# Performance work log

Measured on AMD Instinct MI355X. Metric: run time of the kernel, lower is better.

The kernel has to match this reference:

```python
import jax, jax.numpy as jnp
import numpy as np

B, N, H, DH, E, D_IN = 2, 2048, 8, 32, 65536, 256
O = H * DH
SCALE = float(np.sqrt(DH))


def setup_inputs() -> dict:
    key = jax.random.key(0)
    ks = jax.random.split(key, 8)
    rng = np.random.default_rng(0)
    x = jax.random.normal(ks[0], (B, N, D_IN), jnp.float32)
    adj = jax.random.uniform(ks[1], (B, N, N), jnp.float32)
    # unique edges per graph so scatter-add matches torch advanced-index +=
    flat = np.stack([rng.choice(N * N, size=E, replace=False) for _ in range(B)])
    edge_index = jnp.asarray(np.stack([flat // N, flat % N], axis=1), jnp.int32)  # [B,2,E]
    edge_attr = jax.random.normal(ks[2], (B, E, H), jnp.float32)
    mask = jnp.ones((B, N), dtype=bool)
    qkv_w = jax.random.normal(ks[3], (D_IN, 3 * O), jnp.float32) / np.sqrt(D_IN)
    qkv_b = jnp.zeros((3 * O,), jnp.float32)
    e_w1 = jax.random.normal(ks[4], (H, H), jnp.float32) / np.sqrt(H)
    e_b1 = jnp.zeros((H,), jnp.float32)
    e_w2 = jax.random.normal(ks[5], (H, H), jnp.float32) / np.sqrt(H)
    e_b2 = jnp.zeros((H,), jnp.float32)
    shifts = jnp.asarray(np.linspace(0.1, 0.8, H), jnp.float32).reshape(1, H, 1, 1)
    widths = jnp.full((1, H, 1, 1), 0.5, jnp.float32)
    self_loop_W = jnp.asarray(1.0 / DH + rng.uniform(0, 1, H), jnp.float32).reshape(1, H, 1, 1)
    return dict(x=x, adj=adj, edge_attr=edge_attr, qkv_w=qkv_w, qkv_b=qkv_b,
                e_w1=e_w1, e_b1=e_b1, e_w2=e_w2, e_b2=e_b2,
                shifts=shifts, widths=widths, self_loop_W=self_loop_W,
                edge_index=edge_index, mask=mask)


def reference(x, adj, edge_attr, qkv_w, qkv_b, e_w1, e_b1, e_w2, e_b2,
              shifts, widths, self_loop_W, edge_index, mask):
    Bq, Nq = x.shape[0], x.shape[1]
    # qkv projection -> [3,B,H,N,DH]
    qkv = (x @ qkv_w + qkv_b).reshape(Bq, Nq, 3, H, DH)
    qkv = jnp.transpose(qkv, (2, 0, 3, 1, 4))
    Q, K, V = qkv[0], qkv[1], qkv[2]
    # edge FFN applied twice (eval mode: noise/dropout are identity)
    def ffn(e):
        return jax.nn.relu(e @ e_w1 + e_b1) @ e_w2 + e_b2
    ea = ffn(ffn(edge_attr))                      # [B,E,H]
    ea = jnp.transpose(ea, (0, 2, 1))             # [B,H,E]
    # scores + learned moire adjacency bias
    scores = jnp.einsum('bhqd,bhkd->bhqk', Q, K) / SCALE
    moire = jnp.exp(-((adj[:, None] - shifts) ** 2) / (2.0 * widths ** 2))  # gaussian focus
    moire = jnp.clip(moire, 1e-6, None)
    s = scores + jnp.log(moire)                   # [B,H,N,N]
    # scatter edge features into score matrix
    u = edge_index[:, 0, :]                        # [B,E]
    v = edge_index[:, 1, :]
    bi = jnp.arange(Bq)[:, None, None]
    hi = jnp.arange(H)[None, :, None]
    s = s.at[bi, hi, u[:, None, :], v[:, None, :]].add(ea)
    # self-loop diagonal bias (non-trainable)
    s = s + jnp.eye(Nq, dtype=s.dtype)[None, None] * self_loop_W
    # mask and softmax
    m2 = mask[:, None, :] & mask[:, :, None]       # [B,N,N]
    s = jnp.where(m2[:, None], s, jnp.asarray(-1e6, s.dtype))
    attn = jax.nn.softmax(s, axis=-1)
    out = jnp.einsum('bhqk,bhkd->bhqd', attn, V)
    return jnp.transpose(out, (0, 2, 1, 3)).reshape(Bq, Nq, O)
```

## Files before the change

kernel.cpp:

```cpp
#include <hip/hip_runtime.h>

#define B_ 2
#define N_ 2048
#define H_ 8
#define DH_ 32
#define E_ 65536
#define DIN_ 256
#define KT 256
#define PAD 4
#define ECAP 32
#define INV_SCALE 0.17677669529663687f
#define LOGMIN -13.815510557964274f

typedef short bf16x8 __attribute__((ext_vector_type(8)));
typedef float floatx4 __attribute__((ext_vector_type(4)));

__device__ __forceinline__ unsigned short f2b(float f){
  union { float f; unsigned int u; } v; v.f = f;
  return (unsigned short)((v.u + 0x7fffu + ((v.u >> 16) & 1u)) >> 16);
}
__device__ __forceinline__ bf16x8 f8_to_bf(const float* p){
  float4 a = *(const float4*)p, b = *(const float4*)(p + 4);
  bf16x8 r;
  r[0] = (short)f2b(a.x); r[1] = (short)f2b(a.y); r[2] = (short)f2b(a.z); r[3] = (short)f2b(a.w);
  r[4] = (short)f2b(b.x); r[5] = (short)f2b(b.y); r[6] = (short)f2b(b.z); r[7] = (short)f2b(b.w);
  return r;
}

__global__ __launch_bounds__(256) void prep_kernel(
    const float* __restrict__ eattr,
    const float* __restrict__ w1, const float* __restrict__ b1,
    const float* __restrict__ w2, const float* __restrict__ b2,
    float* __restrict__ ea,
    const int* __restrict__ ei, int* __restrict__ cnt, unsigned int* __restrict__ pck,
    const float* __restrict__ w, unsigned short* __restrict__ wT)
{
  int bb = blockIdx.x, tid = threadIdx.x;
  if (bb < 512){
    __shared__ float W1[64], W2[64], Bv1[8], Bv2[8];
    if (tid < 64){ W1[tid] = w1[tid]; W2[tid] = w2[tid]; }
    if (tid < 8){ Bv1[tid] = b1[tid]; Bv2[tid] = b2[tid]; }
    __syncthreads();
    int gid = bb * 256 + tid;
    const float* ep = eattr + (size_t)gid * 8;
    float cur[8];
#pragma unroll
    for (int i = 0; i < 8; ++i) cur[i] = ep[i];
#pragma unroll
    for (int pass = 0; pass < 2; ++pass){
      float t[8];
#pragma unroll
      for (int j = 0; j < 8; ++j){
        float s = Bv1[j];
#pragma unroll
        for (int i = 0; i < 8; ++i) s += cur[i] * W1[i * 8 + j];
        t[j] = fmaxf(s, 0.f);
      }
#pragma unroll
      for (int j = 0; j < 8; ++j){
        float s = Bv2[j];
#pragma unroll
        for (int i = 0; i < 8; ++i) s += t[i] * W2[i * 8 + j];
        cur[j] = s;
      }
    }
    float* op = ea + (size_t)gid * 8;
#pragma unroll
    for (int j = 0; j < 8; ++j) op[j] = cur[j];
  } else if (bb < 1024){
    int gid = (bb - 512) * 256 + tid;
    int b = gid >> 16, e = gid & (E_ - 1);
    int u = ei[(size_t)b * 2 * E_ + e];
    int v = ei[(size_t)b * 2 * E_ + E_ + e];
    int bucket = ((b << 11) + u) * 8 + (v >> 8);
    int slot = atomicAdd(&cnt[bucket], 1);
    if (slot < ECAP) pck[(size_t)bucket * ECAP + slot] = ((unsigned int)e << 11) | (unsigned int)v;
  } else {
    int k = bb - 1024;
    for (int c = tid; c < 768; c += 256)
      wT[(size_t)c * 256 + k] = f2b(w[(size_t)k * 768 + c]);
  }
}

__global__ __launch_bounds__(256) void qkv_kernel(
    const float* __restrict__ x, const unsigned short* __restrict__ wT,
    const float* __restrict__ bias,
    unsigned short* __restrict__ Qb, unsigned short* __restrict__ Kb, unsigned short* __restrict__ Vt)
{
  int tid = threadIdx.x;
  int wave = tid >> 6, lane = tid & 63, m = lane & 15, quad = lane >> 4;
  int rowbase = blockIdx.x * 16;
  int colbase = blockIdx.y * 64 + wave * 16;
  floatx4 acc = {0.f, 0.f, 0.f, 0.f};
#pragma unroll
  for (int kb = 0; kb < 8; ++kb){
    bf16x8 af = f8_to_bf(x + (size_t)(rowbase + m) * DIN_ + kb * 32 + quad * 8);
    bf16x8 bf = *(const bf16x8*)(wT + (size_t)(colbase + m) * DIN_ + kb * 32 + quad * 8);
    acc = __builtin_amdgcn_mfma_f32_16x16x32_bf16(af, bf, acc, 0, 0, 0);
  }
  int ccol = colbase + m;
  int which = ccol >> 8, hh = (ccol >> 5) & 7, dh = ccol & 31;
  float bv = bias[ccol];
#pragma unroll
  for (int r = 0; r < 4; ++r){
    int row = rowbase + quad * 4 + r;
    int bidx = row >> 11, n = row & (N_ - 1);
    float val = acc[r] + bv;
    size_t bh = (size_t)(bidx * H_ + hh);
    if (which == 0)      Qb[(bh * N_ + n) * DH_ + dh] = f2b(val * INV_SCALE);
    else if (which == 1) Kb[(bh * N_ + n) * DH_ + dh] = f2b(val);
    else                 Vt[(bh * DH_ + dh) * N_ + n] = f2b(val);
  }
}

__global__ __launch_bounds__(256) void attn_kernel(
    const unsigned short* __restrict__ Qb, const unsigned short* __restrict__ Kb,
    const unsigned short* __restrict__ Vt, const float* __restrict__ adj,
    const float* __restrict__ ea, const int* __restrict__ cnt, const unsigned int* __restrict__ pck,
    const float* __restrict__ shifts, const float* __restrict__ widths,
    const float* __restrict__ selfW, float* __restrict__ out)
{
  __shared__ float S[16][KT + PAD];
  __shared__ float mpart[4][16];
  __shared__ float mrowW[4][16];
  __shared__ float arowW[4][16];
  __shared__ float lfin[4][16];

  int bid = blockIdx.x;
  int qt = bid & 127, h = (bid >> 7) & 7, b = bid >> 10;
  int qbase = qt * 16;
  int tid = threadIdx.x, wave = tid >> 6, lane = tid & 63, m = lane & 15, quad = lane >> 4;
  float shift_h = shifts[h];
  float w_h = widths[h];
  float i2w_h = 1.f / (2.f * w_h * w_h);
  float selfW_h = selfW[h];
  size_t krow = (size_t)(b * H_ + h) * N_;
  size_t vrow = (size_t)(b * H_ + h) * DH_;
  bf16x8 qfrag = *(const bf16x8*)(Qb + (krow + qbase + m) * DH_ + quad * 8);

  float mcur = -1e30f;
  float lcur = 0.f;
  floatx4 oacc0 = {0.f, 0.f, 0.f, 0.f};
  floatx4 oacc1 = {0.f, 0.f, 0.f, 0.f};

  for (int kt = 0; kt < N_ / KT; ++kt){
    int k0 = kt * KT;
    bool diagtile = (k0 == (qbase & ~(KT - 1)));
#pragma unroll
    for (int s = 0; s < 4; ++s){
      int colofs = wave * 64 + s * 16;
      bf16x8 kf = *(const bf16x8*)(Kb + (krow + k0 + colofs + m) * DH_ + quad * 8);
      floatx4 acc = {0.f, 0.f, 0.f, 0.f};
      acc = __builtin_amdgcn_mfma_f32_16x16x32_bf16(qfrag, kf, acc, 0, 0, 0);
      int t = colofs + m - (qbase - k0);
#pragma unroll
      for (int r = 0; r < 4; ++r){
        float v = acc[r];
        if (diagtile && t == quad * 4 + r) v += selfW_h;
        S[quad * 4 + r][colofs + m] = v;
      }
    }
    __syncthreads();
#pragma unroll
    for (int ii = 0; ii < 4; ++ii){
      int i = tid + ii * 256;
      int r = i >> 6, c4 = (i & 63) << 2;
      float4 av = *(const float4*)(adj + ((size_t)b * N_ + qbase + r) * N_ + k0 + c4);
      float4* sp = (float4*)&S[r][c4];
      float4 sv = *sp;
      float d;
      d = av.x - shift_h; sv.x += fmaxf(-d * d * i2w_h, LOGMIN);
      d = av.y - shift_h; sv.y += fmaxf(-d * d * i2w_h, LOGMIN);
      d = av.z - shift_h; sv.z += fmaxf(-d * d * i2w_h, LOGMIN);
      d = av.w - shift_h; sv.w += fmaxf(-d * d * i2w_h, LOGMIN);
      *sp = sv;
    }
    __syncthreads();
#pragma unroll
    for (int ii = 0; ii < 2; ++ii){
      int i = tid + ii * 256;
      int r = i >> 5, slot = i & (ECAP - 1);
      int bucket = (b * N_ + qbase + r) * 8 + kt;
      int nb = cnt[bucket]; nb = nb > ECAP ? ECAP : nb;
      if (slot < nb){
        unsigned int p = pck[(size_t)bucket * ECAP + slot];
        int vv = (int)(p & (N_ - 1));
        int e  = (int)(p >> 11);
        S[r][vv - k0] += ea[((size_t)b * E_ + e) * H_ + h];
      }
    }
    __syncthreads();
    const float* sp0 = &S[m][wave * 64 + quad * 8];
    float4 s00 = *(const float4*)(sp0);
    float4 s01 = *(const float4*)(sp0 + 4);
    float4 s10 = *(const float4*)(sp0 + 32);
    float4 s11 = *(const float4*)(sp0 + 36);
    bf16x8 vf00 = *(const bf16x8*)(Vt + (vrow + m) * N_      + k0 + wave * 64 + quad * 8);
    bf16x8 vf01 = *(const bf16x8*)(Vt + (vrow + 16 + m) * N_ + k0 + wave * 64 + quad * 8);
    bf16x8 vf10 = *(const bf16x8*)(Vt + (vrow + m) * N_      + k0 + wave * 64 + 32 + quad * 8);
    bf16x8 vf11 = *(const bf16x8*)(Vt + (vrow + 16 + m) * N_ + k0 + wave * 64 + 32 + quad * 8);
    float lm = fmaxf(fmaxf(fmaxf(s00.x, s00.y), fmaxf(s00.z, s00.w)),
                     fmaxf(fmaxf(s01.x, s01.y), fmaxf(s01.z, s01.w)));
    lm = fmaxf(lm, fmaxf(fmaxf(fmaxf(s10.x, s10.y), fmaxf(s10.z, s10.w)),
                         fmaxf(fmaxf(s11.x, s11.y), fmaxf(s11.z, s11.w))));
    lm = fmaxf(lm, __shfl_xor(lm, 16));
    lm = fmaxf(lm, __shfl_xor(lm, 32));
    if (quad == 0) mpart[wave][m] = lm;
    __syncthreads();
    if (lane < 16){
      float tmax = fmaxf(fmaxf(mpart[0][lane], mpart[1][lane]),
                         fmaxf(mpart[2][lane], mpart[3][lane]));
      float mnew = fmaxf(mcur, tmax);
      float al = __expf(mcur - mnew);
      mcur = mnew;
      mrowW[wave][lane] = mnew;
      arowW[wave][lane] = al;
    }
    __threadfence_block();
    float mr  = mrowW[wave][m];
    float alA = arowW[wave][m];
    float4 aq = *(const float4*)&arowW[wave][quad * 4];
    oacc0[0] *= aq.x; oacc0[1] *= aq.y; oacc0[2] *= aq.z; oacc0[3] *= aq.w;
    oacc1[0] *= aq.x; oacc1[1] *= aq.y; oacc1[2] *= aq.z; oacc1[3] *= aq.w;
    float ps = 0.f, p;
    bf16x8 pf;
    p = __expf(s00.x - mr); ps += p; pf[0] = (short)f2b(p);
    p = __expf(s00.y - mr); ps += p; pf[1] = (short)f2b(p);
    p = __expf(s00.z - mr); ps += p; pf[2] = (short)f2b(p);
    p = __expf(s00.w - mr); ps += p; pf[3] = (short)f2b(p);
    p = __expf(s01.x - mr); ps += p; pf[4] = (short)f2b(p);
    p = __expf(s01.y - mr); ps += p; pf[5] = (short)f2b(p);
    p = __expf(s01.z - mr); ps += p; pf[6] = (short)f2b(p);
    p = __expf(s01.w - mr); ps += p; pf[7] = (short)f2b(p);
    oacc0 = __builtin_amdgcn_mfma_f32_16x16x32_bf16(pf, vf00, oacc0, 0, 0, 0);
    oacc1 = __builtin_amdgcn_mfma_f32_16x16x32_bf16(pf, vf01, oacc1, 0, 0, 0);
    p = __expf(s10.x - mr); ps += p; pf[0] = (short)f2b(p);
    p = __expf(s10.y - mr); ps += p; pf[1] = (short)f2b(p);
    p = __expf(s10.z - mr); ps += p; pf[2] = (short)f2b(p);
    p = __expf(s10.w - mr); ps += p; pf[3] = (short)f2b(p);
    p = __expf(s11.x - mr); ps += p; pf[4] = (short)f2b(p);
    p = __expf(s11.y - mr); ps += p; pf[5] = (short)f2b(p);
    p = __expf(s11.z - mr); ps += p; pf[6] = (short)f2b(p);
    p = __expf(s11.w - mr); ps += p; pf[7] = (short)f2b(p);
    oacc0 = __builtin_amdgcn_mfma_f32_16x16x32_bf16(pf, vf10, oacc0, 0, 0, 0);
    oacc1 = __builtin_amdgcn_mfma_f32_16x16x32_bf16(pf, vf11, oacc1, 0, 0, 0);
    ps += __shfl_xor(ps, 16);
    ps += __shfl_xor(ps, 32);
    lcur = lcur * alA + ps;
  }

  float* Op = &S[0][0];
#pragma unroll
  for (int r = 0; r < 4; ++r){
    Op[(wave * 16 + quad * 4 + r) * 32 + m]      = oacc0[r];
    Op[(wave * 16 + quad * 4 + r) * 32 + 16 + m] = oacc1[r];
  }
  if (lane < 16) lfin[wave][lane] = lcur;
  __syncthreads();
#pragma unroll
  for (int ii = 0; ii < 2; ++ii){
    int i = tid + ii * 256;
    int r = i >> 5, d = i & 31;
    float o = Op[r * 32 + d] + Op[(16 + r) * 32 + d] + Op[(32 + r) * 32 + d] + Op[(48 + r) * 32 + d];
    float l = lfin[0][r] + lfin[1][r] + lfin[2][r] + lfin[3][r];
    out[((size_t)b * N_ + qbase + r) * (H_ * DH_) + h * DH_ + d] = o / l;
  }
}

extern "C" void kernel_launch(void* const* d_in, const int* in_sizes, int n_in,
                              void* d_out, int out_size, void* d_ws, size_t ws_size,
                              hipStream_t stream)
{
  const float* x      = (const float*)d_in[0];
  const float* adj    = (const float*)d_in[1];
  const float* eattr  = (const float*)d_in[2];
  const float* qkvw   = (const float*)d_in[3];
  const float* qkvb   = (const float*)d_in[4];
  const float* ew1    = (const float*)d_in[5];
  const float* eb1    = (const float*)d_in[6];
  const float* ew2    = (const float*)d_in[7];
  const float* eb2    = (const float*)d_in[8];
  const float* shifts = (const float*)d_in[9];
  const float* widths = (const float*)d_in[10];
  const float* selfW  = (const float*)d_in[11];
  const int*   ei     = (const int*)d_in[12];
  float* out = (float*)d_out;

  char* ws = (char*)d_ws;
  unsigned short* Qb  = (unsigned short*)(ws);
  unsigned short* Kb  = (unsigned short*)(ws + ((size_t)2 << 20));
  unsigned short* Vt  = (unsigned short*)(ws + ((size_t)4 << 20));
  unsigned short* wT  = (unsigned short*)(ws + ((size_t)6 << 20));
  float*          ea  = (float*)(ws + ((size_t)7 << 20));
  int*            cnt = (int*)(ws + ((size_t)11 << 20));
  unsigned int*  pck  = (unsigned int*)(ws + ((size_t)12 << 20));

  hipMemsetAsync(cnt, 0, (size_t)B_ * N_ * 8 * sizeof(int), stream);
  hipLaunchKernelGGL(prep_kernel, dim3(1280), dim3(256), 0, stream,
                     eattr, ew1, eb1, ew2, eb2, ea, ei, cnt, pck, qkvw, wT);
  hipLaunchKernelGGL(qkv_kernel, dim3(256, 12), dim3(256), 0, stream, x, wT, qkvb, Qb, Kb, Vt);
  hipLaunchKernelGGL(attn_kernel, dim3(B_ * H_ * (N_ / 16)), dim3(256), 0, stream,
                     Qb, Kb, Vt, adj, ea, cnt, pck, shifts, widths, selfW, out);
}
```

Baseline: 247.1 us.

## Make attention waves independent with per-wave softmax state and exp2 math

Each wave now keeps its own 64-column slice of the score tile, its own running max and sum, and its own scatter of edge features. This removes the block-wide barriers inside the key loop, and the four partial results are merged once at the end with max-rescaling. The adjacency bias is computed in registers instead of through shared memory. Scores are carried in the log2 domain so exp2 can be used, with LOG2E folded into the Q scale, the edge features and the self-loop weight, and P is packed to bf16 with v_cvt_pk_bf16_f32. The edge scatter now has each wave scan all bucket slots and filter to its own columns, which repeats the loads across the four waves, and it relies on s_waitcnt in place of barriers for LDS ordering.

```diff
diff --git a/kernel.cpp b/kernel.cpp
--- a/kernel.cpp
+++ b/kernel.cpp
@@ -7,10 +7,10 @@
 #define E_ 65536
 #define DIN_ 256
 #define KT 256
-#define PAD 4
 #define ECAP 32
-#define INV_SCALE 0.17677669529663687f
-#define LOGMIN -13.815510557964274f
+#define QSCALE 0.2550348872f
+#define LOG2E 1.4426950408889634f
+#define LOG2MIN -19.931568569324174f
 
 typedef short bf16x8 __attribute__((ext_vector_type(8)));
 typedef float floatx4 __attribute__((ext_vector_type(4)));
@@ -24,6 +24,11 @@
   bf16x8 r;
   r[0] = (short)f2b(a.x); r[1] = (short)f2b(a.y); r[2] = (short)f2b(a.z); r[3] = (short)f2b(a.w);
   r[4] = (short)f2b(b.x); r[5] = (short)f2b(b.y); r[6] = (short)f2b(b.z); r[7] = (short)f2b(b.w);
+  return r;
+}
+__device__ __forceinline__ unsigned int cvt_pk_bf16(float lo, float hi){
+  unsigned int r;
+  asm("v_cvt_pk_bf16_f32 %0, %1, %2" : "=v"(r) : "v"(lo), "v"(hi));
   return r;
 }
 
@@ -66,7 +71,7 @@
     }
     float* op = ea + (size_t)gid * 8;
 #pragma unroll
-    for (int j = 0; j < 8; ++j) op[j] = cur[j];
+    for (int j = 0; j < 8; ++j) op[j] = cur[j] * LOG2E;
   } else if (bb < 1024){
     int gid = (bb - 512) * 256 + tid;
     int b = gid >> 16, e = gid & (E_ - 1);
@@ -101,15 +106,22 @@
   int ccol = colbase + m;
   int which = ccol >> 8, hh = (ccol >> 5) & 7, dh = ccol & 31;
   float bv = bias[ccol];
-#pragma unroll
-  for (int r = 0; r < 4; ++r){
-    int row = rowbase + quad * 4 + r;
-    int bidx = row >> 11, n = row & (N_ - 1);
-    float val = acc[r] + bv;
-    size_t bh = (size_t)(bidx * H_ + hh);
-    if (which == 0)      Qb[(bh * N_ + n) * DH_ + dh] = f2b(val * INV_SCALE);
-    else if (which == 1) Kb[(bh * N_ + n) * DH_ + dh] = f2b(val);
-    else                 Vt[(bh * DH_ + dh) * N_ + n] = f2b(val);
+  int row0 = rowbase + quad * 4;
+  int bidx = row0 >> 11, n0 = row0 & (N_ - 1);
+  size_t bh = (size_t)(bidx * H_ + hh);
+  if (which == 0){
+#pragma unroll
+    for (int r = 0; r < 4; ++r)
+      Qb[(bh * N_ + n0 + r) * DH_ + dh] = f2b((acc[r] + bv) * QSCALE);
+  } else if (which == 1){
+#pragma unroll
+    for (int r = 0; r < 4; ++r)
+      Kb[(bh * N_ + n0 + r) * DH_ + dh] = f2b(acc[r] + bv);
+  } else {
+    ushort4 st;
+    st.x = f2b(acc[0] + bv); st.y = f2b(acc[1] + bv);
+    st.z = f2b(acc[2] + bv); st.w = f2b(acc[3] + bv);
+    *(ushort4*)(Vt + (bh * DH_ + dh) * N_ + n0) = st;
   }
 }
 
@@ -120,11 +132,8 @@
     const float* __restrict__ shifts, const float* __restrict__ widths,
     const float* __restrict__ selfW, float* __restrict__ out)
 {
-  __shared__ float S[16][KT + PAD];
-  __shared__ float mpart[4][16];
-  __shared__ float mrowW[4][16];
-  __shared__ float arowW[4][16];
-  __shared__ float lfin[4][16];
+  __shared__ float S[4][16][68];
+  __shared__ float mfin[4][16], lfin[4][16];
 
   int bid = blockIdx.x;
   int qt = bid & 127, h = (bid >> 7) & 7, b = bid >> 10;
@@ -132,138 +141,144 @@
   int tid = threadIdx.x, wave = tid >> 6, lane = tid & 63, m = lane & 15, quad = lane >> 4;
   float shift_h = shifts[h];
   float w_h = widths[h];
-  float i2w_h = 1.f / (2.f * w_h * w_h);
-  float selfW_h = selfW[h];
+  float i2w_h = LOG2E / (2.f * w_h * w_h);
+  float selfW_h = selfW[h] * LOG2E;
   size_t krow = (size_t)(b * H_ + h) * N_;
   size_t vrow = (size_t)(b * H_ + h) * DH_;
   bf16x8 qfrag = *(const bf16x8*)(Qb + (krow + qbase + m) * DH_ + quad * 8);
-
-  float mcur = -1e30f;
-  float lcur = 0.f;
+  float (*Sw)[68] = S[wave];
+
+  int rr = lane >> 2, sl0 = lane & 3;
+  const int* cntp = cnt + ((size_t)(b * N_) + qbase + rr) * 8;
+  const unsigned int* pckp = pck + ((size_t)((b * N_ + qbase + rr) * 8)) * ECAP;
+  const float* eabase = ea + (size_t)b * E_ * H_ + h;
+  const float* adjp = adj + ((size_t)b * N_ + qbase + m) * N_ + wave * 64 + quad * 8;
+  const unsigned short* vp0 = Vt + (vrow + m) * N_ + wave * 64 + quad * 8;
+  const unsigned short* vp1 = Vt + (vrow + 16 + m) * N_ + wave * 64 + quad * 8;
+  const unsigned short* kp  = Kb + (krow + wave * 64 + m) * DH_ + quad * 8;
+
+  float mcur = -1e30f, lcur = 0.f;
   floatx4 oacc0 = {0.f, 0.f, 0.f, 0.f};
   floatx4 oacc1 = {0.f, 0.f, 0.f, 0.f};
 
   for (int kt = 0; kt < N_ / KT; ++kt){
     int k0 = kt * KT;
-    bool diagtile = (k0 == (qbase & ~(KT - 1)));
+    int dq = qbase - k0 - wave * 64;
 #pragma unroll
     for (int s = 0; s < 4; ++s){
-      int colofs = wave * 64 + s * 16;
-      bf16x8 kf = *(const bf16x8*)(Kb + (krow + k0 + colofs + m) * DH_ + quad * 8);
+      bf16x8 kf = *(const bf16x8*)(kp + (size_t)(k0 + s * 16) * DH_);
       floatx4 acc = {0.f, 0.f, 0.f, 0.f};
       acc = __builtin_amdgcn_mfma_f32_16x16x32_bf16(qfrag, kf, acc, 0, 0, 0);
-      int t = colofs + m - (qbase - k0);
+      int t = s * 16 + m - dq;
 #pragma unroll
       for (int r = 0; r < 4; ++r){
         float v = acc[r];
-        if (diagtile && t == quad * 4 + r) v += selfW_h;
-        S[quad * 4 + r][colofs + m] = v;
+        if (t == quad * 4 + r) v += selfW_h;
+        Sw[quad * 4 + r][s * 16 + m] = v;
       }
     }
-    __syncthreads();
-#pragma unroll
-    for (int ii = 0; ii < 4; ++ii){
-      int i = tid + ii * 256;
-      int r = i >> 6, c4 = (i & 63) << 2;
-      float4 av = *(const float4*)(adj + ((size_t)b * N_ + qbase + r) * N_ + k0 + c4);
-      float4* sp = (float4*)&S[r][c4];
-      float4 sv = *sp;
-      float d;
-      d = av.x - shift_h; sv.x += fmaxf(-d * d * i2w_h, LOGMIN);
-      d = av.y - shift_h; sv.y += fmaxf(-d * d * i2w_h, LOGMIN);
-      d = av.z - shift_h; sv.z += fmaxf(-d * d * i2w_h, LOGMIN);
-      d = av.w - shift_h; sv.w += fmaxf(-d * d * i2w_h, LOGMIN);
-      *sp = sv;
-    }
-    __syncthreads();
-#pragma unroll
-    for (int ii = 0; ii < 2; ++ii){
-      int i = tid + ii * 256;
-      int r = i >> 5, slot = i & (ECAP - 1);
-      int bucket = (b * N_ + qbase + r) * 8 + kt;
-      int nb = cnt[bucket]; nb = nb > ECAP ? ECAP : nb;
-      if (slot < nb){
-        unsigned int p = pck[(size_t)bucket * ECAP + slot];
-        int vv = (int)(p & (N_ - 1));
-        int e  = (int)(p >> 11);
-        S[r][vv - k0] += ea[((size_t)b * E_ + e) * H_ + h];
+    asm volatile("s_waitcnt lgkmcnt(0)" ::: "memory");
+    {
+      int nb = cntp[kt]; nb = nb > ECAP ? ECAP : nb;
+      const unsigned int* pb = pckp + kt * ECAP;
+      for (int slot = sl0; slot < nb; slot += 4){
+        unsigned int pk = pb[slot];
+        int vv = (int)(pk & (unsigned int)(N_ - 1));
+        int c = vv - k0 - wave * 64;
+        if ((unsigned)c < 64u){
+          int e = (int)(pk >> 11);
+          Sw[rr][c] += eabase[(size_t)e * H_];
+        }
       }
     }
-    __syncthreads();
-    const float* sp0 = &S[m][wave * 64 + quad * 8];
-    float4 s00 = *(const float4*)(sp0);
-    float4 s01 = *(const float4*)(sp0 + 4);
-    float4 s10 = *(const float4*)(sp0 + 32);
-    float4 s11 = *(const float4*)(sp0 + 36);
-    bf16x8 vf00 = *(const bf16x8*)(Vt + (vrow + m) * N_      + k0 + wave * 64 + quad * 8);
-    bf16x8 vf01 = *(const bf16x8*)(Vt + (vrow + 16 + m) * N_ + k0 + wave * 64 + quad * 8);
-    bf16x8 vf10 = *(const bf16x8*)(Vt + (vrow + m) * N_      + k0 + wave * 64 + 32 + quad * 8);
-    bf16x8 vf11 = *(const bf16x8*)(Vt + (vrow + 16 + m) * N_ + k0 + wave * 64 + 32 + quad * 8);
+    asm volatile("s_waitcnt lgkmcnt(0)" ::: "memory");
+    const float* sp = &Sw[m][quad * 8];
+    float4 s00 = *(const float4*)(sp);
+    float4 s01 = *(const float4*)(sp + 4);
+    float4 s10 = *(const float4*)(sp + 32);
+    float4 s11 = *(const float4*)(sp + 36);
+    const float* ap = adjp + k0;
+    float4 a00 = *(const float4*)(ap);
+    float4 a01 = *(const float4*)(ap + 4);
+    float4 a10 = *(const float4*)(ap + 32);
+    float4 a11 = *(const float4*)(ap + 36);
+    bf16x8 vf00 = *(const bf16x8*)(vp0 + k0);
+    bf16x8 vf01 = *(const bf16x8*)(vp1 + k0);
+    bf16x8 vf10 = *(const bf16x8*)(vp0 + k0 + 32);
+    bf16x8 vf11 = *(const bf16x8*)(vp1 + k0 + 32);
+    float dd;
+    dd = a00.x - shift_h; s00.x += fmaxf(-dd * dd * i2w_h, LOG2MIN);
+    dd = a00.y - shift_h; s00.y += fmaxf(-dd * dd * i2w_h, LOG2MIN);
+    dd = a00.z - shift_h; s00.z += fmaxf(-dd * dd * i2w_h, LOG2MIN);
+    dd = a00.w - shift_h; s00.w += fmaxf(-dd * dd * i2w_h, LOG2MIN);
+    dd = a01.x - shift_h; s01.x += fmaxf(-dd * dd * i2w_h, LOG2MIN);
+    dd = a01.y - shift_h; s01.y += fmaxf(-dd * dd * i2w_h, LOG2MIN);
+    dd = a01.z - shift_h; s01.z += fmaxf(-dd * dd * i2w_h, LOG2MIN);
+    dd = a01.w - shift_h; s01.w += fmaxf(-dd * dd * i2w_h, LOG2MIN);
+    dd = a10.x - shift_h; s10.x += fmaxf(-dd * dd * i2w_h, LOG2MIN);
+    dd = a10.y - shift_h; s10.y += fmaxf(-dd * dd * i2w_h, LOG2MIN);
+    dd = a10.z - shift_h; s10.z += fmaxf(-dd * dd * i2w_h, LOG2MIN);
+    dd = a10.w - shift_h; s10.w += fmaxf(-dd * dd * i2w_h, LOG2MIN);
+    dd = a11.x - shift_h; s11.x += fmaxf(-dd * dd * i2w_h, LOG2MIN);
+    dd = a11.y - shift_h; s11.y += fmaxf(-dd * dd * i2w_h, LOG2MIN);
+    dd = a11.z - shift_h; s11.z += fmaxf(-dd * dd * i2w_h, LOG2MIN);
+    dd = a11.w - shift_h; s11.w += fmaxf(-dd * dd * i2w_h, LOG2MIN);
     float lm = fmaxf(fmaxf(fmaxf(s00.x, s00.y), fmaxf(s00.z, s00.w)),
                      fmaxf(fmaxf(s01.x, s01.y), fmaxf(s01.z, s01.w)));
     lm = fmaxf(lm, fmaxf(fmaxf(fmaxf(s10.x, s10.y), fmaxf(s10.z, s10.w)),
                          fmaxf(fmaxf(s11.x, s11.y), fmaxf(s11.z, s11.w))));
     lm = fmaxf(lm, __shfl_xor(lm, 16));
     lm = fmaxf(lm, __shfl_xor(lm, 32));
-    if (quad == 0) mpart[wave][m] = lm;
-    __syncthreads();
-    if (lane < 16){
-      float tmax = fmaxf(fmaxf(mpart[0][lane], mpart[1][lane]),
-                         fmaxf(mpart[2][lane], mpart[3][lane]));
-      float mnew = fmaxf(mcur, tmax);
-      float al = __expf(mcur - mnew);
-      mcur = mnew;
-      mrowW[wave][lane] = mnew;
-      arowW[wave][lane] = al;
-    }
-    __threadfence_block();
-    float mr  = mrowW[wave][m];
-    float alA = arowW[wave][m];
-    float4 aq = *(const float4*)&arowW[wave][quad * 4];
-    oacc0[0] *= aq.x; oacc0[1] *= aq.y; oacc0[2] *= aq.z; oacc0[3] *= aq.w;
-    oacc1[0] *= aq.x; oacc1[1] *= aq.y; oacc1[2] *= aq.z; oacc1[3] *= aq.w;
-    float ps = 0.f, p;
-    bf16x8 pf;
-    p = __expf(s00.x - mr); ps += p; pf[0] = (short)f2b(p);
-    p = __expf(s00.y - mr); ps += p; pf[1] = (short)f2b(p);
-    p = __expf(s00.z - mr); ps += p; pf[2] = (short)f2b(p);
-    p = __expf(s00.w - mr); ps += p; pf[3] = (short)f2b(p);
-    p = __expf(s01.x - mr); ps += p; pf[4] = (short)f2b(p);
-    p = __expf(s01.y - mr); ps += p; pf[5] = (short)f2b(p);
-    p = __expf(s01.z - mr); ps += p; pf[6] = (short)f2b(p);
-    p = __expf(s01.w - mr); ps += p; pf[7] = (short)f2b(p);
-    oacc0 = __builtin_amdgcn_mfma_f32_16x16x32_bf16(pf, vf00, oacc0, 0, 0, 0);
-    oacc1 = __builtin_amdgcn_mfma_f32_16x16x32_bf16(pf, vf01, oacc1, 0, 0, 0);
-    p = __expf(s10.x - mr); ps += p; pf[0] = (short)f2b(p);
-    p = __expf(s10.y - mr); ps += p; pf[1] = (short)f2b(p);
-    p = __expf(s10.z - mr); ps += p; pf[2] = (short)f2b(p);
-    p = __expf(s10.w - mr); ps += p; pf[3] = (short)f2b(p);
-    p = __expf(s11.x - mr); ps += p; pf[4] = (short)f2b(p);
-    p = __expf(s11.y - mr); ps += p; pf[5] = (short)f2b(p);
-    p = __expf(s11.z - mr); ps += p; pf[6] = (short)f2b(p);
-    p = __expf(s11.w - mr); ps += p; pf[7] = (short)f2b(p);
-    oacc0 = __builtin_amdgcn_mfma_f32_16x16x32_bf16(pf, vf10, oacc0, 0, 0, 0);
-    oacc1 = __builtin_amdgcn_mfma_f32_16x16x32_bf16(pf, vf11, oacc1, 0, 0, 0);
+    float mnew = fmaxf(mcur, lm);
+    float al = exp2f(mcur - mnew);
+    mcur = mnew;
+    float al0 = __shfl(al, quad * 4 + 0);
+    float al1 = __shfl(al, quad * 4 + 1);
+    float al2 = __shfl(al, quad * 4 + 2);
+    float al3 = __shfl(al, quad * 4 + 3);
+    oacc0[0] *= al0; oacc0[1] *= al1; oacc0[2] *= al2; oacc0[3] *= al3;
+    oacc1[0] *= al0; oacc1[1] *= al1; oacc1[2] *= al2; oacc1[3] *= al3;
+    float ps = 0.f, p0, p1;
+    union { bf16x8 v; unsigned int u[4]; } P;
+    p0 = exp2f(s00.x - mcur); p1 = exp2f(s00.y - mcur); ps += p0 + p1; P.u[0] = cvt_pk_bf16(p0, p1);
+    p0 = exp2f(s00.z - mcur); p1 = exp2f(s00.w - mcur); ps += p0 + p1; P.u[1] = cvt_pk_bf16(p0, p1);
+    p0 = exp2f(s01.x - mcur); p1 = exp2f(s01.y - mcur); ps += p0 + p1; P.u[2] = cvt_pk_bf16(p0, p1);
+    p0 = exp2f(s01.z - mcur); p1 = exp2f(s01.w - mcur); ps += p0 + p1; P.u[3] = cvt_pk_bf16(p0, p1);
+    oacc0 = __builtin_amdgcn_mfma_f32_16x16x32_bf16(P.v, vf00, oacc0, 0, 0, 0);
+    oacc1 = __builtin_amdgcn_mfma_f32_16x16x32_bf16(P.v, vf01, oacc1, 0, 0, 0);
+    p0 = exp2f(s10.x - mcur); p1 = exp2f(s10.y - mcur); ps += p0 + p1; P.u[0] = cvt_pk_bf16(p0, p1);
+    p0 = exp2f(s10.z - mcur); p1 = exp2f(s10.w - mcur); ps += p0 + p1; P.u[1] = cvt_pk_bf16(p0, p1);
+    p0 = exp2f(s11.x - mcur); p1 = exp2f(s11.y - mcur); ps += p0 + p1; P.u[2] = cvt_pk_bf16(p0, p1);
+    p0 = exp2f(s11.z - mcur); p1 = exp2f(s11.w - mcur); ps += p0 + p1; P.u[3] = cvt_pk_bf16(p0, p1);
+    oacc0 = __builtin_amdgcn_mfma_f32_16x16x32_bf16(P.v, vf10, oacc0, 0, 0, 0);
+    oacc1 = __builtin_amdgcn_mfma_f32_16x16x32_bf16(P.v, vf11, oacc1, 0, 0, 0);
     ps += __shfl_xor(ps, 16);
     ps += __shfl_xor(ps, 32);
-    lcur = lcur * alA + ps;
-  }
-
-  float* Op = &S[0][0];
+    lcur = lcur * al + ps;
+  }
+
+  if (quad == 0){ mfin[wave][m] = mcur; lfin[wave][m] = lcur; }
+  float* Ow = &S[wave][0][0];
 #pragma unroll
   for (int r = 0; r < 4; ++r){
-    Op[(wave * 16 + quad * 4 + r) * 32 + m]      = oacc0[r];
-    Op[(wave * 16 + quad * 4 + r) * 32 + 16 + m] = oacc1[r];
-  }
-  if (lane < 16) lfin[wave][lane] = lcur;
+    Ow[(quad * 4 + r) * 32 + m]      = oacc0[r];
+    Ow[(quad * 4 + r) * 32 + 16 + m] = oacc1[r];
+  }
   __syncthreads();
+  const float* Sv = &S[0][0][0];
 #pragma unroll
   for (int ii = 0; ii < 2; ++ii){
     int i = tid + ii * 256;
-    int r = i >> 5, d = i & 31;
-    float o = Op[r * 32 + d] + Op[(16 + r) * 32 + d] + Op[(32 + r) * 32 + d] + Op[(48 + r) * 32 + d];
-    float l = lfin[0][r] + lfin[1][r] + lfin[2][r] + lfin[3][r];
-    out[((size_t)b * N_ + qbase + r) * (H_ * DH_) + h * DH_ + d] = o / l;
+    int r = i >> 5, dcol = i & 31;
+    float m0 = mfin[0][r], m1 = mfin[1][r], m2 = mfin[2][r], m3 = mfin[3][r];
+    float mg = fmaxf(fmaxf(m0, m1), fmaxf(m2, m3));
+    float w0 = exp2f(m0 - mg), w1 = exp2f(m1 - mg);
+    float w2 = exp2f(m2 - mg), w3 = exp2f(m3 - mg);
+    int o_idx = r * 32 + dcol;
+    float o = Sv[o_idx] * w0 + Sv[1088 + o_idx] * w1
+            + Sv[2176 + o_idx] * w2 + Sv[3264 + o_idx] * w3;
+    float l = lfin[0][r] * w0 + lfin[1][r] * w1 + lfin[2][r] * w2 + lfin[3][r] * w3;
+    out[((size_t)b * N_ + qbase + r) * (H_ * DH_) + h * DH_ + dcol] = o / l;
   }
 }
 
```

After: 234.3 us. 1.05x faster.
